# Kernel optimization log

Hardware: AMD Instinct MI355X
Metric: run time of the kernel (lower is better)

The kernel has to match this reference:

```python
import jax, jax.numpy as jnp
import numpy as np

NUM_WIRES = 14
LAYERS = 3
PPL = 3
BATCH = 1024
DIM = 2 ** NUM_WIRES


def setup_inputs() -> dict:
    key = jax.random.key(0)
    k1, k2, k3, k4, k5 = jax.random.split(key, 5)
    sr = jax.random.normal(k1, (BATCH, DIM), jnp.float32)
    si = jax.random.normal(k2, (BATCH, DIM), jnp.float32)
    norm = jnp.sqrt(jnp.sum(sr * sr + si * si, axis=1, keepdims=True))
    sr, si = sr / norm, si / norm  # normalized amplitude-encoded states
    weights = jax.random.normal(k3, (LAYERS, PPL, NUM_WIRES), jnp.float32)
    head_w = jax.random.normal(k4, (1, NUM_WIRES), jnp.float32) / np.sqrt(NUM_WIRES)
    head_b = jax.random.normal(k5, (1,), jnp.float32) * 0.01
    return {"state_real": sr, "state_imag": si, "weights": weights,
            "head_w": head_w, "head_b": head_b}


def _apply_ry_all(st, angles):
    # st: (B,)+(2,)*n complex; apply RY(angles[q]) on each wire q (RYs on distinct wires commute)
    half = angles * 0.5
    c, s = jnp.cos(half), jnp.sin(half)
    for q in range(NUM_WIRES):
        ax = 1 + q
        a0 = jnp.take(st, 0, axis=ax)
        a1 = jnp.take(st, 1, axis=ax)
        n0 = c[q] * a0 - s[q] * a1
        n1 = s[q] * a0 + c[q] * a1
        st = jnp.stack([n0, n1], axis=ax)
    return st


def _apply_cnot(st, ctrl, tgt):
    # flip target axis only where control bit == 1
    ctrl_ax, tgt_ax = 1 + ctrl, 1 + tgt
    flipped = jnp.flip(st, axis=tgt_ax)
    mask_shape = [1] * (NUM_WIRES + 1)
    mask_shape[ctrl_ax] = 2
    mask = (jnp.arange(2).reshape(mask_shape) == 1)
    return jnp.where(mask, flipped, st)


def _circuit(state, weights):
    # state: (B, DIM) complex64 -> PauliZ expvals (B, NUM_WIRES)
    st = state.reshape((-1,) + (2,) * NUM_WIRES)
    for l in range(LAYERS):
        # sequential RY(w[l,p,q]) for p=0..PPL-1 on wire q compose to RY(sum_p w[l,p,q])
        ang = jnp.sum(weights[l], axis=0)  # (NUM_WIRES,)
        st = _apply_ry_all(st, ang)
        for j in range(NUM_WIRES):
            st = _apply_cnot(st, j, (j + 1) % NUM_WIRES)
    probs = st.real ** 2 + st.imag ** 2  # (B,)+(2,)*n
    probs = probs.reshape(-1, DIM)
    idx = jnp.arange(DIM)
    # PennyLane convention: wire 0 is the most significant bit
    bits = (idx[None, :] >> (NUM_WIRES - 1 - jnp.arange(NUM_WIRES))[:, None]) & 1  # (n, DIM)
    signs = (1 - 2 * bits).astype(probs.dtype)
    return probs @ signs.T  # (B, n)


def reference(state_real, state_imag, weights, head_w, head_b):
    state = jax.lax.complex(state_real, state_imag)
    feats = _circuit(state, weights)  # (B, NUM_WIRES)
    return feats @ head_w[0] + head_b[0]  # (B,)
```

## Files before the change

### kernel.cpp

```cpp
#include <hip/hip_runtime.h>

typedef unsigned int u32;

#define DIM 16384
#define NT  512

__host__ __device__ constexpr u32 swz0(u32 d) {
    u32 b1 = ((d >> 4) ^ (d >> 5) ^ (d >> 8)) & 1u;
    u32 b2 = (d >> 6) & 1u;
    u32 b3 = (d >> 7) & 1u;
    return d ^ (b1 << 1) ^ (b2 << 2) ^ (b3 << 3);
}

__host__ __device__ constexpr u32 mmap(u32 y) {
    u32 s = y;
    s ^= s >> 1; s ^= s >> 2; s ^= s >> 4; s ^= s >> 8;
    return (s & 0x1FFFu) | (((s ^ (y >> 13)) & 1u) << 13);
}

__device__ __forceinline__ void rot(float& a0, float& a1, float c, float s) {
    float n0 = fmaf(c, a0, -(s * a1));
    float n1 = fmaf(s, a0,  (c * a1));
    a0 = n0; a1 = n1;
}

template<int L, int P>
__device__ __forceinline__ void doPass(int tid, float* smem, float (&re)[32], float (&im)[32],
                                       float& acc, float W0)
{
    float2* st2 = (float2*)smem;
    const float* angC  = smem + 32768;
    const float* angS  = smem + 32768 + 48;
    const float* lutLo = smem + 32768 + 96;
    const float* lutHi = smem + 32768 + 96 + 128;

    constexpr int HB = (P == 0) ? 11 : (P == 1) ? 8 : (P == 2) ? 5 : 2;
    u32 t = (u32)tid;
    u32 ybase =
        (P == 0) ? (t << 2) :
        (P == 1) ? (((t & 63u) << 2) | ((t >> 6) << 11)) :
        (P == 2) ? (((t & 7u)  << 2) | ((t >> 3) << 8)) :
                   (t << 5);
    u32 sbase = swz0(ybase);

    if (!(L == 0 && P == 0)) {
        const float4* stv = (const float4*)st2;
        #pragma unroll
        for (int h = 0; h < 8; ++h) {
            #pragma unroll
            for (int m = 0; m < 2; ++m) {
                u32 idx = (sbase ^ swz0(((u32)h << HB) | ((u32)m << 1))) >> 1;
                float4 v = stv[idx];
                int r = h * 4 + m * 2;
                re[r] = v.x; im[r] = v.y; re[r + 1] = v.z; im[r + 1] = v.w;
            }
        }
    }

    #pragma unroll
    for (int i = 0; i < 3; ++i) {
        float c = angC[L * 16 + HB + i];
        float s = angS[L * 16 + HB + i];
        #pragma unroll
        for (int hh = 0; hh < 8; ++hh) {
            if (hh & (1 << i)) continue;
            #pragma unroll
            for (int k = 0; k < 4; ++k) {
                int r0 = hh * 4 + k, r1 = (hh | (1 << i)) * 4 + k;
                rot(re[r0], re[r1], c, s);
                rot(im[r0], im[r1], c, s);
            }
        }
    }
    if (P == 0) {
        float c1 = angC[L * 16 + 1], s1 = angS[L * 16 + 1];
        #pragma unroll
        for (int hh = 0; hh < 8; ++hh) {
            #pragma unroll
            for (int k = 0; k < 2; ++k) {
                int r0 = hh * 4 + k;
                rot(re[r0], re[r0 + 2], c1, s1);
                rot(im[r0], im[r0 + 2], c1, s1);
            }
        }
        float c0 = angC[L * 16 + 0], s0 = angS[L * 16 + 0];
        #pragma unroll
        for (int hh = 0; hh < 8; ++hh) {
            #pragma unroll
            for (int k = 0; k < 4; k += 2) {
                int r0 = hh * 4 + k;
                rot(re[r0], re[r0 + 1], c0, s0);
                rot(im[r0], im[r0 + 1], c0, s0);
            }
        }
    }

    if (P < 3) {
        float4* stv = (float4*)st2;
        #pragma unroll
        for (int h = 0; h < 8; ++h) {
            #pragma unroll
            for (int m = 0; m < 2; ++m) {
                u32 idx = (sbase ^ swz0(((u32)h << HB) | ((u32)m << 1))) >> 1;
                int r = h * 4 + m * 2;
                stv[idx] = make_float4(re[r], im[r], re[r + 1], im[r + 1]);
            }
        }
        __syncthreads();
    } else if (L < 2) {
        __syncthreads();
        u32 pbase = swz0(mmap(ybase));
        #pragma unroll
        for (int h = 0; h < 8; ++h) {
            #pragma unroll
            for (int k = 0; k < 4; ++k) {
                u32 slot = pbase ^ swz0(mmap(((u32)h << 2) | (u32)k));
                int r = h * 4 + k;
                st2[slot] = make_float2(re[r], im[r]);
            }
        }
        __syncthreads();
    } else {
        u32 myb = mmap(ybase);
        #pragma unroll
        for (int h = 0; h < 8; ++h) {
            #pragma unroll
            for (int k = 0; k < 4; ++k) {
                u32 yp = myb ^ mmap(((u32)h << 2) | (u32)k);
                int r = h * 4 + k;
                float p  = fmaf(re[r], re[r], im[r] * im[r]);
                float wv = W0 - 2.0f * (lutLo[yp & 127u] + lutHi[yp >> 7]);
                acc = fmaf(wv, p, acc);
            }
        }
    }
}

__global__ __launch_bounds__(NT, 2) void qsim_kernel(
    const float* __restrict__ sreal, const float* __restrict__ simag,
    const float* __restrict__ wts,   const float* __restrict__ hw,
    const float* __restrict__ hb,    float* __restrict__ out)
{
    extern __shared__ float smem[];
    float* angC   = smem + 32768;
    float* angS   = angC + 48;
    float* lutLo  = angS + 48;
    float* lutHi  = lutLo + 128;
    float* redbuf = lutHi + 128;

    int tid = threadIdx.x;
    int b   = blockIdx.x;

    const float4* pr = (const float4*)(sreal + (size_t)b * DIM);
    const float4* pi = (const float4*)(simag + (size_t)b * DIM);
    float4 vr[8], vi[8];
    #pragma unroll
    for (int h = 0; h < 8; ++h) {
        vr[h] = pr[(h << 9) | tid];
        vi[h] = pi[(h << 9) | tid];
    }

    if (tid < 42) {
        int l = tid / 14, bb = tid % 14, q = 13 - bb;
        float a = 0.5f * (wts[l * 42 + q] + wts[l * 42 + 14 + q] + wts[l * 42 + 28 + q]);
        angC[l * 16 + bb] = cosf(a);
        angS[l * 16 + bb] = sinf(a);
    } else if (tid >= 64 && tid < 192) {
        int i = tid - 64;
        float ssum = 0.f;
        for (int bb = 0; bb < 7; ++bb) if ((i >> bb) & 1) ssum += hw[13 - bb];
        lutLo[i] = ssum;
    } else if (tid >= 192 && tid < 320) {
        int i = tid - 192;
        float ssum = 0.f;
        for (int bb = 0; bb < 7; ++bb) if ((i >> bb) & 1) ssum += hw[6 - bb];
        lutHi[i] = ssum;
    }

    float re[32], im[32];
    #pragma unroll
    for (int h = 0; h < 8; ++h) {
        re[h * 4 + 0] = vr[h].x; re[h * 4 + 1] = vr[h].y;
        re[h * 4 + 2] = vr[h].z; re[h * 4 + 3] = vr[h].w;
        im[h * 4 + 0] = vi[h].x; im[h * 4 + 1] = vi[h].y;
        im[h * 4 + 2] = vi[h].z; im[h * 4 + 3] = vi[h].w;
    }

    __syncthreads();
    float W0  = lutLo[127] + lutHi[127];
    float acc = 0.f;

    doPass<0, 0>(tid, smem, re, im, acc, W0);
    doPass<0, 1>(tid, smem, re, im, acc, W0);
    doPass<0, 2>(tid, smem, re, im, acc, W0);
    doPass<0, 3>(tid, smem, re, im, acc, W0);
    doPass<1, 0>(tid, smem, re, im, acc, W0);
    doPass<1, 1>(tid, smem, re, im, acc, W0);
    doPass<1, 2>(tid, smem, re, im, acc, W0);
    doPass<1, 3>(tid, smem, re, im, acc, W0);
    doPass<2, 0>(tid, smem, re, im, acc, W0);
    doPass<2, 1>(tid, smem, re, im, acc, W0);
    doPass<2, 2>(tid, smem, re, im, acc, W0);
    doPass<2, 3>(tid, smem, re, im, acc, W0);

    #pragma unroll
    for (int off = 32; off > 0; off >>= 1) acc += __shfl_xor(acc, off, 64);
    if ((tid & 63) == 0) redbuf[tid >> 6] = acc;
    __syncthreads();
    if (tid == 0) {
        float tot = hb[0];
        #pragma unroll
        for (int i = 0; i < 8; ++i) tot += redbuf[i];
        out[b] = tot;
    }
}

extern "C" void kernel_launch(void* const* d_in, const int* in_sizes, int n_in,
                              void* d_out, int out_size, void* d_ws, size_t ws_size,
                              hipStream_t stream)
{
    const float* sreal = (const float*)d_in[0];
    const float* simag = (const float*)d_in[1];
    const float* wts   = (const float*)d_in[2];
    const float* hw    = (const float*)d_in[3];
    const float* hb    = (const float*)d_in[4];
    float* out = (float*)d_out;

    int batch = in_sizes[0] / DIM;
    size_t smem_bytes = (32768 + 48 + 48 + 128 + 128 + 16) * sizeof(float);

    (void)hipFuncSetAttribute((const void*)qsim_kernel,
                              hipFuncAttributeMaxDynamicSharedMemorySize, (int)smem_bytes);
    qsim_kernel<<<dim3(batch), dim3(NT), smem_bytes, stream>>>(sreal, simag, wts, hw, hb, out);
}
```

Measured before the change: 218.8 us.

## Regroup qubit gates into three LDS passes per layer instead of four

Each layer's 14 RY rotations are now split into three register-resident passes of 5, 5 and 4 wires rather than four passes of 3 or 5 wires. This cuts one LDS store/load round trip and one barrier per layer. The LDS swizzle function is redefined so the new strided access patterns (including float2 accesses at stride 64) avoid bank conflicts. The risk is that the new swizzle still conflicts for some access pattern, or that the scalar float2 accesses in pass B cost more than the float4 accesses they replace.

```diff
diff --git a/kernel.cpp b/kernel.cpp
--- a/kernel.cpp
+++ b/kernel.cpp
@@ -6,9 +6,9 @@
 #define NT  512
 
 __host__ __device__ constexpr u32 swz0(u32 d) {
-    u32 b1 = ((d >> 4) ^ (d >> 5) ^ (d >> 8)) & 1u;
-    u32 b2 = (d >> 6) & 1u;
-    u32 b3 = (d >> 7) & 1u;
+    u32 b1 = (d >> 4) & 1u;
+    u32 b2 = (d >> 7) & 1u;
+    u32 b3 = ((d >> 6) ^ (d >> 8)) & 1u;
     return d ^ (b1 << 1) ^ (b2 << 2) ^ (b3 << 3);
 }
 
@@ -24,98 +24,107 @@
     a0 = n0; a1 = n1;
 }
 
-template<int L, int P>
-__device__ __forceinline__ void doPass(int tid, float* smem, float (&re)[32], float (&im)[32],
-                                       float& acc, float W0)
-{
+template<int D>
+__device__ __forceinline__ void gate32(float (&re)[32], float (&im)[32], float c, float s) {
+    #pragma unroll
+    for (int r = 0; r < 32; ++r) if (!(r & D)) {
+        rot(re[r], re[r | D], c, s);
+        rot(im[r], im[r | D], c, s);
+    }
+}
+
+template<int L>
+__device__ __forceinline__ void passA(int tid, float* smem, float (&re)[32], float (&im)[32]) {
+    float4* stv = (float4*)smem;
+    const float* angC = smem + 32768;
+    const float* angS = smem + 32768 + 48;
+    u32 sbase = swz0((u32)tid << 2);
+    if (L > 0) {
+        #pragma unroll
+        for (int h = 0; h < 8; ++h) {
+            #pragma unroll
+            for (int m = 0; m < 2; ++m) {
+                u32 idx = (sbase ^ swz0(((u32)h << 11) | ((u32)m << 1))) >> 1;
+                float4 v = stv[idx];
+                int r = h * 4 + m * 2;
+                re[r] = v.x; im[r] = v.y; re[r + 1] = v.z; im[r + 1] = v.w;
+            }
+        }
+    }
+    gate32<16>(re, im, angC[L * 16 + 13], angS[L * 16 + 13]);
+    gate32< 8>(re, im, angC[L * 16 + 12], angS[L * 16 + 12]);
+    gate32< 4>(re, im, angC[L * 16 + 11], angS[L * 16 + 11]);
+    gate32< 2>(re, im, angC[L * 16 +  1], angS[L * 16 +  1]);
+    gate32< 1>(re, im, angC[L * 16 +  0], angS[L * 16 +  0]);
+    #pragma unroll
+    for (int h = 0; h < 8; ++h) {
+        #pragma unroll
+        for (int m = 0; m < 2; ++m) {
+            u32 idx = (sbase ^ swz0(((u32)h << 11) | ((u32)m << 1))) >> 1;
+            int r = h * 4 + m * 2;
+            stv[idx] = make_float4(re[r], im[r], re[r + 1], im[r + 1]);
+        }
+    }
+    __syncthreads();
+}
+
+template<int L>
+__device__ __forceinline__ void passB(int tid, float* smem, float (&re)[32], float (&im)[32]) {
     float2* st2 = (float2*)smem;
+    const float* angC = smem + 32768;
+    const float* angS = smem + 32768 + 48;
+    u32 ybase = ((u32)tid & 63u) | (((u32)tid >> 6) << 11);
+    u32 sbase = swz0(ybase);
+    #pragma unroll
+    for (int j = 0; j < 32; ++j) {
+        u32 slot = sbase ^ swz0((u32)j << 6);
+        float2 v = st2[slot];
+        re[j] = v.x; im[j] = v.y;
+    }
+    gate32< 1>(re, im, angC[L * 16 +  6], angS[L * 16 +  6]);
+    gate32< 2>(re, im, angC[L * 16 +  7], angS[L * 16 +  7]);
+    gate32< 4>(re, im, angC[L * 16 +  8], angS[L * 16 +  8]);
+    gate32< 8>(re, im, angC[L * 16 +  9], angS[L * 16 +  9]);
+    gate32<16>(re, im, angC[L * 16 + 10], angS[L * 16 + 10]);
+    #pragma unroll
+    for (int j = 0; j < 32; ++j) {
+        u32 slot = sbase ^ swz0((u32)j << 6);
+        st2[slot] = make_float2(re[j], im[j]);
+    }
+    __syncthreads();
+}
+
+template<int L>
+__device__ __forceinline__ void passC(int tid, float* smem, float (&re)[32], float (&im)[32],
+                                      float& acc, float W0) {
+    float2* st2 = (float2*)smem;
+    float4* stv = (float4*)smem;
     const float* angC  = smem + 32768;
     const float* angS  = smem + 32768 + 48;
     const float* lutLo = smem + 32768 + 96;
     const float* lutHi = smem + 32768 + 96 + 128;
-
-    constexpr int HB = (P == 0) ? 11 : (P == 1) ? 8 : (P == 2) ? 5 : 2;
-    u32 t = (u32)tid;
-    u32 ybase =
-        (P == 0) ? (t << 2) :
-        (P == 1) ? (((t & 63u) << 2) | ((t >> 6) << 11)) :
-        (P == 2) ? (((t & 7u)  << 2) | ((t >> 3) << 8)) :
-                   (t << 5);
+    u32 ybase = (((u32)tid & 1u) << 1) | (((u32)tid >> 1) << 6);
     u32 sbase = swz0(ybase);
-
-    if (!(L == 0 && P == 0)) {
-        const float4* stv = (const float4*)st2;
-        #pragma unroll
-        for (int h = 0; h < 8; ++h) {
-            #pragma unroll
-            for (int m = 0; m < 2; ++m) {
-                u32 idx = (sbase ^ swz0(((u32)h << HB) | ((u32)m << 1))) >> 1;
-                float4 v = stv[idx];
-                int r = h * 4 + m * 2;
-                re[r] = v.x; im[r] = v.y; re[r + 1] = v.z; im[r + 1] = v.w;
-            }
-        }
-    }
-
-    #pragma unroll
-    for (int i = 0; i < 3; ++i) {
-        float c = angC[L * 16 + HB + i];
-        float s = angS[L * 16 + HB + i];
-        #pragma unroll
-        for (int hh = 0; hh < 8; ++hh) {
-            if (hh & (1 << i)) continue;
-            #pragma unroll
-            for (int k = 0; k < 4; ++k) {
-                int r0 = hh * 4 + k, r1 = (hh | (1 << i)) * 4 + k;
-                rot(re[r0], re[r1], c, s);
-                rot(im[r0], im[r1], c, s);
-            }
-        }
-    }
-    if (P == 0) {
-        float c1 = angC[L * 16 + 1], s1 = angS[L * 16 + 1];
-        #pragma unroll
-        for (int hh = 0; hh < 8; ++hh) {
-            #pragma unroll
-            for (int k = 0; k < 2; ++k) {
-                int r0 = hh * 4 + k;
-                rot(re[r0], re[r0 + 2], c1, s1);
-                rot(im[r0], im[r0 + 2], c1, s1);
-            }
-        }
-        float c0 = angC[L * 16 + 0], s0 = angS[L * 16 + 0];
-        #pragma unroll
-        for (int hh = 0; hh < 8; ++hh) {
-            #pragma unroll
-            for (int k = 0; k < 4; k += 2) {
-                int r0 = hh * 4 + k;
-                rot(re[r0], re[r0 + 1], c0, s0);
-                rot(im[r0], im[r0 + 1], c0, s0);
-            }
-        }
-    }
-
-    if (P < 3) {
-        float4* stv = (float4*)st2;
-        #pragma unroll
-        for (int h = 0; h < 8; ++h) {
-            #pragma unroll
-            for (int m = 0; m < 2; ++m) {
-                u32 idx = (sbase ^ swz0(((u32)h << HB) | ((u32)m << 1))) >> 1;
-                int r = h * 4 + m * 2;
-                stv[idx] = make_float4(re[r], im[r], re[r + 1], im[r + 1]);
-            }
-        }
-        __syncthreads();
-    } else if (L < 2) {
+    #pragma unroll
+    for (int h = 0; h < 16; ++h) {
+        u32 idx = (sbase ^ swz0((u32)h << 2)) >> 1;
+        float4 v = stv[idx];
+        int r = h * 2;
+        re[r] = v.x; im[r] = v.y; re[r + 1] = v.z; im[r + 1] = v.w;
+    }
+    gate32< 2>(re, im, angC[L * 16 + 2], angS[L * 16 + 2]);
+    gate32< 4>(re, im, angC[L * 16 + 3], angS[L * 16 + 3]);
+    gate32< 8>(re, im, angC[L * 16 + 4], angS[L * 16 + 4]);
+    gate32<16>(re, im, angC[L * 16 + 5], angS[L * 16 + 5]);
+    if (L < 2) {
         __syncthreads();
         u32 pbase = swz0(mmap(ybase));
         #pragma unroll
-        for (int h = 0; h < 8; ++h) {
+        for (int h = 0; h < 16; ++h) {
             #pragma unroll
-            for (int k = 0; k < 4; ++k) {
-                u32 slot = pbase ^ swz0(mmap(((u32)h << 2) | (u32)k));
-                int r = h * 4 + k;
+            for (int q = 0; q < 2; ++q) {
+                u32 slot = pbase ^ swz0(mmap(((u32)h << 2) | (u32)q));
+                int r = h * 2 + q;
                 st2[slot] = make_float2(re[r], im[r]);
             }
         }
@@ -123,11 +132,11 @@
     } else {
         u32 myb = mmap(ybase);
         #pragma unroll
-        for (int h = 0; h < 8; ++h) {
+        for (int h = 0; h < 16; ++h) {
             #pragma unroll
-            for (int k = 0; k < 4; ++k) {
-                u32 yp = myb ^ mmap(((u32)h << 2) | (u32)k);
-                int r = h * 4 + k;
+            for (int q = 0; q < 2; ++q) {
+                u32 yp = myb ^ mmap(((u32)h << 2) | (u32)q);
+                int r = h * 2 + q;
                 float p  = fmaf(re[r], re[r], im[r] * im[r]);
                 float wv = W0 - 2.0f * (lutLo[yp & 127u] + lutHi[yp >> 7]);
                 acc = fmaf(wv, p, acc);
@@ -190,18 +199,15 @@
     float W0  = lutLo[127] + lutHi[127];
     float acc = 0.f;
 
-    doPass<0, 0>(tid, smem, re, im, acc, W0);
-    doPass<0, 1>(tid, smem, re, im, acc, W0);
-    doPass<0, 2>(tid, smem, re, im, acc, W0);
-    doPass<0, 3>(tid, smem, re, im, acc, W0);
-    doPass<1, 0>(tid, smem, re, im, acc, W0);
-    doPass<1, 1>(tid, smem, re, im, acc, W0);
-    doPass<1, 2>(tid, smem, re, im, acc, W0);
-    doPass<1, 3>(tid, smem, re, im, acc, W0);
-    doPass<2, 0>(tid, smem, re, im, acc, W0);
-    doPass<2, 1>(tid, smem, re, im, acc, W0);
-    doPass<2, 2>(tid, smem, re, im, acc, W0);
-    doPass<2, 3>(tid, smem, re, im, acc, W0);
+    passA<0>(tid, smem, re, im);
+    passB<0>(tid, smem, re, im);
+    passC<0>(tid, smem, re, im, acc, W0);
+    passA<1>(tid, smem, re, im);
+    passB<1>(tid, smem, re, im);
+    passC<1>(tid, smem, re, im, acc, W0);
+    passA<2>(tid, smem, re, im);
+    passB<2>(tid, smem, re, im);
+    passC<2>(tid, smem, re, im, acc, W0);
 
     #pragma unroll
     for (int off = 32; off > 0; off >>= 1) acc += __shfl_xor(acc, off, 64);
```

After: 210.5 us. 3.8% less time.
